# Kernel optimization log

Measured on AMD Instinct MI355X. Metric: run time of the kernel, lower is better.

Reference implementation:

```python
import jax, jax.numpy as jnp
import numpy as np

N, E, M, G = 100000, 1600000, 20000, 512
IN, ED, OUT, H, C = 64, 16, 64, 4, 8


def segment_softmax(alpha, seg, num):
    # alpha: [Etot, H]; softmax over edges sharing the same destination segment
    amax = jax.ops.segment_max(alpha, seg, num_segments=num)
    amax = jnp.where(jnp.isneginf(amax), 0.0, amax)
    ex = jnp.exp(alpha - amax[seg])
    den = jax.ops.segment_sum(ex, seg, num_segments=num)
    return ex / (den[seg] + 1e-16)


def gat_conv(x, src, dst, ea, W, We, a_s, a_d, a_e, b, concat):
    # PyG GATConv: shared lin for src/dst, edge-conditioned attention, self loops pre-added
    n = x.shape[0]
    h, c = a_s.shape
    hx = (x @ W).reshape(n, h, c)            # [N,H,C]
    ee = (ea @ We).reshape(-1, h, c)          # [Etot,H,C]
    alpha = jax.nn.leaky_relu((hx * a_s).sum(-1)[src] + (hx * a_d).sum(-1)[dst] + (ee * a_e).sum(-1), 0.2)
    alpha = segment_softmax(alpha, dst, n)    # [Etot,H]
    out = jax.ops.segment_sum(hx[src] * alpha[:, :, None], dst, num_segments=n)
    out = out.reshape(n, h * c) if concat else out.mean(axis=1)
    return out + b


def setup_inputs() -> dict:
    keys = iter(jax.random.split(jax.random.key(0), 64))

    def nrm(shape, s=0.1):
        return jax.random.normal(next(keys), shape, jnp.float32) * s

    inp = {}
    inp["x"] = jax.random.normal(next(keys), (N, IN), jnp.float32)
    inp["edge_index"] = jax.random.randint(next(keys), (2, E), 0, N)
    inp["edge_attr"] = jax.random.normal(next(keys), (E, ED), jnp.float32)
    inp["scatter_index"] = jax.random.randint(next(keys), (N,), 0, M)
    inp["scatter_norm"] = jax.random.uniform(next(keys), (M, 1), jnp.float32, 0.5, 2.0)
    inp["nodes"] = jax.random.randint(next(keys), (M,), 0, G)
    inp["decision_var_indexes"] = jax.random.randint(next(keys), (G,), 0, N)
    dims = [(IN, H, C), (H * C, H, C), (H * C, H, C), (H * C, H, OUT)]
    for i, (din, hh, cc) in enumerate(dims, 1):
        inp[f"W{i}"] = nrm((din, hh * cc))
        inp[f"We{i}"] = nrm((ED, hh * cc))
        inp[f"asrc{i}"] = nrm((hh, cc))
        inp[f"adst{i}"] = nrm((hh, cc))
        inp[f"ae{i}"] = nrm((hh, cc))
        inp[f"b{i}"] = nrm((hh * cc if i < 4 else cc,))
    inp["Wp"] = nrm((OUT, OUT))
    inp["Wt"] = nrm((OUT, OUT))
    inp["Wo"] = nrm((2 * OUT, 1))
    inp["bo"] = nrm((1,))
    return inp


def reference(x, edge_index, edge_attr, scatter_index, scatter_norm, nodes, decision_var_indexes,
              W1, We1, asrc1, adst1, ae1, b1, W2, We2, asrc2, adst2, ae2, b2,
              W3, We3, asrc3, adst3, ae3, b3, W4, We4, asrc4, adst4, ae4, b4,
              Wp, Wt, Wo, bo):
    # add self loops once; edge_attr fill_value='mean' (PyG GATConv default)
    loop = jnp.arange(N)
    src = jnp.concatenate([edge_index[0], loop])
    dst = jnp.concatenate([edge_index[1], loop])
    ea = jnp.concatenate([edge_attr, jnp.broadcast_to(edge_attr.mean(0), (N, ED))], 0)
    lrelu = lambda v: jax.nn.leaky_relu(v, 0.01)
    h1 = lrelu(gat_conv(x, src, dst, ea, W1, We1, asrc1, adst1, ae1, b1, True))
    h2 = lrelu(gat_conv(h1, src, dst, ea, W2, We2, asrc2, adst2, ae2, b2, True))
    h3 = lrelu(gat_conv(h2, src, dst, ea, W3, We3, asrc3, adst3, ae3, b3, True))
    h4 = lrelu(gat_conv(h3, src, dst, ea, W4, We4, asrc4, adst4, ae4, b4, False))
    pool = jax.ops.segment_sum(h4, scatter_index, num_segments=M) / scatter_norm
    pool = jax.ops.segment_sum(pool, nodes, num_segments=G)   # [G,OUT]
    tgt = h4[decision_var_indexes]                             # [G,OUT]
    feat = lrelu(jnp.concatenate([pool @ Wp, tgt @ Wt], axis=1))
    return feat @ Wo + bo
```

## Files before the change

kernel.cpp:

```cpp
#include <hip/hip_runtime.h>
#include <math.h>

#define NN 100000
#define EE 1600000
#define ETOT 1700000
#define MM 20000
#define GG 512

#define NBUCK 782
#define NB1 256
#define CAP 4096

static constexpr int NB_N256 = (NN + 255) / 256;
static constexpr int NB_E256 = (ETOT + 255) / 256;
static constexpr int NB_AGG  = NN / 32;

#define SM_MEAN 0
#define SM_WEA 16
#define SM_VS4 272
#define SM_VD4 400
#define SM_W4P 536
#define SM_TOTAL 8728

typedef unsigned long long ull;

__device__ __forceinline__ unsigned short f2bf(float f) {
  unsigned int u = __float_as_uint(f);
  u += 0x7fffu + ((u >> 16) & 1u);
  return (unsigned short)(u >> 16);
}
__device__ __forceinline__ float bf2f(unsigned int h) {
  return __uint_as_float(h << 16);
}
__device__ __forceinline__ float lrelu(float v, float s) { return v > 0.f ? v : s * v; }

__global__ __launch_bounds__(256) void k_pre(
    float* __restrict__ sm, const float* __restrict__ We1, const float* __restrict__ We2,
    const float* __restrict__ We3, const float* __restrict__ We4,
    const float* __restrict__ ae1, const float* __restrict__ ae2,
    const float* __restrict__ ae3, const float* __restrict__ ae4,
    const float* __restrict__ as4, const float* __restrict__ ad4,
    const float* __restrict__ W4) {
  int t = threadIdx.x;
  {
    int l = t >> 6, d = (t >> 2) & 15, h = t & 3;
    const float* We = (l == 0) ? We1 : (l == 1) ? We2 : (l == 2) ? We3 : We4;
    const float* ae = (l == 0) ? ae1 : (l == 1) ? ae2 : (l == 2) ? ae3 : ae4;
    int C = (l == 3) ? 64 : 8;
    float s = 0.f;
    for (int c = 0; c < C; c++) s += We[d * (4 * C) + h * C + c] * ae[h * C + c];
    sm[SM_WEA + l * 64 + d * 4 + h] = s;
  }
  if (t < 128) {
    int k = t >> 2, h = t & 3;
    float s1 = 0.f, s2 = 0.f;
    for (int c = 0; c < 64; c++) {
      float w = W4[k * 256 + h * 64 + c];
      s1 += w * as4[h * 64 + c];
      s2 += w * ad4[h * 64 + c];
    }
    sm[SM_VS4 + t] = s1;
    sm[SM_VD4 + t] = s2;
  }
  for (int i = t; i < 8192; i += 256) {
    int row = i >> 6, c = i & 63;
    int h = row >> 5, k = row & 31;
    sm[SM_W4P + i] = 0.25f * W4[k * 256 + h * 64 + c];
  }
}

__global__ __launch_bounds__(1024) void k_hist1(const int* __restrict__ ei,
                                                const float* __restrict__ ea,
                                                int* __restrict__ blk_cnt,
                                                float* __restrict__ sm) {
  __shared__ int hist[NBUCK];
  __shared__ float lsum[16];
  int t = threadIdx.x;
  for (int i = t; i < NBUCK; i += 1024) hist[i] = 0;
  if (t < 16) lsum[t] = 0.f;
  __syncthreads();
  for (int e = blockIdx.x * 1024 + t; e < ETOT; e += NB1 * 1024) {
    int dst = (e < EE) ? ei[EE + e] : (e - EE);
    atomicAdd(&hist[dst >> 7], 1);
  }
  {
    const float4* ea4 = (const float4*)ea;
    int q = t & 3;
    float4 a = make_float4(0.f, 0.f, 0.f, 0.f);
    for (size_t i = (size_t)blockIdx.x * 1024 + t; i < (size_t)EE * 4;
         i += (size_t)NB1 * 1024) {
      float4 v = ea4[i];
      a.x += v.x; a.y += v.y; a.z += v.z; a.w += v.w;
    }
    for (int m = 4; m < 64; m <<= 1) {
      a.x += __shfl_xor(a.x, m, 64);
      a.y += __shfl_xor(a.y, m, 64);
      a.z += __shfl_xor(a.z, m, 64);
      a.w += __shfl_xor(a.w, m, 64);
    }
    if ((t & 63) < 4) {
      atomicAdd(&lsum[q * 4 + 0], a.x);
      atomicAdd(&lsum[q * 4 + 1], a.y);
      atomicAdd(&lsum[q * 4 + 2], a.z);
      atomicAdd(&lsum[q * 4 + 3], a.w);
    }
  }
  __syncthreads();
  for (int i = t; i < NBUCK; i += 1024) blk_cnt[blockIdx.x * NBUCK + i] = hist[i];
  if (t < 16) atomicAdd(&sm[SM_MEAN + t], lsum[t]);
}

__global__ __launch_bounds__(256) void k_bscan_a(const int* __restrict__ blk_cnt,
                                                 int* __restrict__ blk_base_T,
                                                 int* __restrict__ bucket_tot) {
  __shared__ int s[256];
  int b = blockIdx.x, t = threadIdx.x;
  int v = blk_cnt[t * NBUCK + b];
  s[t] = v;
  __syncthreads();
  for (int off = 1; off < 256; off <<= 1) {
    int x = (t >= off) ? s[t - off] : 0;
    __syncthreads();
    s[t] += x;
    __syncthreads();
  }
  blk_base_T[b * 256 + t] = s[t] - v;
  if (t == 255) bucket_tot[b] = s[255];
}

__global__ __launch_bounds__(1024) void k_bscan_b(const int* __restrict__ bucket_tot,
                                                  int* __restrict__ bucket_base,
                                                  int* __restrict__ row_off) {
  __shared__ int s[1024];
  int t = threadIdx.x;
  int v = (t < NBUCK) ? bucket_tot[t] : 0;
  s[t] = v;
  __syncthreads();
  for (int off = 1; off < 1024; off <<= 1) {
    int x = (t >= off) ? s[t - off] : 0;
    __syncthreads();
    s[t] += x;
    __syncthreads();
  }
  if (t < NBUCK) bucket_base[t] = s[t] - v;
  if (t == 0) {
    bucket_base[NBUCK] = ETOT;
    row_off[NN] = ETOT;
  }
}

__global__ __launch_bounds__(1024) void k_scatter1(const int* __restrict__ ei,
                                                   const int* __restrict__ bucket_base,
                                                   const int* __restrict__ blk_base_T,
                                                   uint2* __restrict__ pairs) {
  __shared__ int base[NBUCK];
  __shared__ int rank[NBUCK];
  int t = threadIdx.x, blk = blockIdx.x;
  for (int i = t; i < NBUCK; i += 1024) {
    base[i] = bucket_base[i] + blk_base_T[i * 256 + blk];
    rank[i] = 0;
  }
  __syncthreads();
  for (int e = blk * 1024 + t; e < ETOT; e += NB1 * 1024) {
    int src, dst;
    if (e < EE) {
      src = ei[e];
      dst = ei[EE + e];
    } else {
      src = dst = e - EE;
    }
    int bin = dst >> 7;
    int r = atomicAdd(&rank[bin], 1);
    pairs[base[bin] + r] =
        make_uint2((unsigned)src, (unsigned)e | ((unsigned)(dst & 127) << 21));
  }
}

__global__ __launch_bounds__(256) void k_sort2(const uint2* __restrict__ pairs,
                                               const int* __restrict__ bucket_base,
                                               int* __restrict__ row_off,
                                               int* __restrict__ csr_src,
                                               int* __restrict__ eidx) {
  __shared__ uint2 plds[CAP];
  __shared__ unsigned short perm[CAP];
  __shared__ int hist[128];
  __shared__ int scan[128];
  __shared__ int rankv[128];
  int b = blockIdx.x, t = threadIdx.x;
  int start = bucket_base[b], end = bucket_base[b + 1];
  int cnt = end - start;
  if (t < 128) hist[t] = 0;
  __syncthreads();
  bool fits = (cnt <= CAP);
  if (fits) {
    for (int i = t; i < cnt; i += 256) {
      uint2 pe = pairs[start + i];
      plds[i] = pe;
      atomicAdd(&hist[(pe.y >> 21) & 127], 1);
    }
  } else {
    for (int i = t; i < cnt; i += 256)
      atomicAdd(&hist[(pairs[start + i].y >> 21) & 127], 1);
  }
  __syncthreads();
  if (t < 128) scan[t] = hist[t];
  __syncthreads();
  for (int off = 1; off < 128; off <<= 1) {
    int x = (t >= off && t < 128) ? scan[t - off] : 0;
    __syncthreads();
    if (t < 128) scan[t] += x;
    __syncthreads();
  }
  if (t < 128) {
    int excl = scan[t] - hist[t];
    rankv[t] = excl;
    int dst = b * 128 + t;
    if (dst < NN) row_off[dst] = start + excl;
  }
  __syncthreads();
  if (fits) {
    for (int i = t; i < cnt; i += 256) {
      int bin = (plds[i].y >> 21) & 127;
      int r = atomicAdd(&rankv[bin], 1);
      perm[r] = (unsigned short)i;
    }
    __syncthreads();
    for (int r = t; r < cnt; r += 256) {
      uint2 pe = plds[perm[r]];
      csr_src[start + r] = (int)pe.x;
      eidx[start + r] = (int)(pe.y & 0x1fffffu);
    }
  } else {
    for (int i = t; i < cnt; i += 256) {
      uint2 pe = pairs[start + i];
      int bin = (pe.y >> 21) & 127;
      int r = atomicAdd(&rankv[bin], 1);
      csr_src[start + r] = (int)pe.x;
      eidx[start + r] = (int)(pe.y & 0x1fffffu);
    }
  }
}

__global__ __launch_bounds__(256) void k_pack(const int* __restrict__ eidx,
                                              const float* __restrict__ ea,
                                              const float* __restrict__ sm,
                                              ull* __restrict__ apc) {
  __shared__ float sWea[256];
  __shared__ float smean[16];
  int t = threadIdx.x;
  sWea[t] = sm[SM_WEA + t];
  if (t < 16) smean[t] = sm[SM_MEAN + t] * (1.f / EE);
  __syncthreads();
  int pos = blockIdx.x * 256 + t;
  if (pos >= ETOT) return;
  int eid = eidx[pos];
  float eav[16];
  if (eid < EE) {
    const float4* p = (const float4*)(ea + (size_t)eid * 16);
    float4 v0 = p[0], v1 = p[1], v2 = p[2], v3 = p[3];
    eav[0] = v0.x; eav[1] = v0.y; eav[2] = v0.z; eav[3] = v0.w;
    eav[4] = v1.x; eav[5] = v1.y; eav[6] = v1.z; eav[7] = v1.w;
    eav[8] = v2.x; eav[9] = v2.y; eav[10] = v2.z; eav[11] = v2.w;
    eav[12] = v3.x; eav[13] = v3.y; eav[14] = v3.z; eav[15] = v3.w;
  } else {
#pragma unroll
    for (int d = 0; d < 16; d++) eav[d] = smean[d];
  }
#pragma unroll
  for (int l = 0; l < 4; l++) {
    ull pk = 0;
#pragma unroll
    for (int h = 0; h < 4; h++) {
      float s = 0.f;
#pragma unroll
      for (int d = 0; d < 16; d++) s += eav[d] * sWea[l * 64 + d * 4 + h];
      pk |= (ull)f2bf(s) << (16 * h);
    }
    apc[(size_t)l * ETOT + pos] = pk;
  }
}

template <int DIN>
__global__ __launch_bounds__(256) void k_t(const float* __restrict__ in,
                                           const float* __restrict__ W,
                                           const float* __restrict__ a_s,
                                           const float* __restrict__ a_d,
                                           unsigned short* __restrict__ hxb,
                                           float* __restrict__ ssrc,
                                           float* __restrict__ sdst) {
  __shared__ float4 sW[DIN * 8];
  __shared__ float sas[32], sad[32];
  int t = threadIdx.x;
  for (int i = t; i < DIN * 8; i += 256) sW[i] = ((const float4*)W)[i];
  if (t < 32) { sas[t] = a_s[t]; sad[t] = a_d[t]; }
  __syncthreads();
  int n = blockIdx.x * 256 + t;
  if (n >= NN) return;
  float acc[32];
#pragma unroll
  for (int j = 0; j < 32; j++) acc[j] = 0.f;
  const float* xr = in + (size_t)n * DIN;
  for (int k = 0; k < DIN; k += 4) {
    float4 xv = *(const float4*)(xr + k);
    float xa[4] = {xv.x, xv.y, xv.z, xv.w};
#pragma unroll
    for (int kk = 0; kk < 4; kk++) {
#pragma unroll
      for (int j4 = 0; j4 < 8; j4++) {
        float4 ww = sW[(k + kk) * 8 + j4];
        acc[j4 * 4 + 0] += xa[kk] * ww.x;
        acc[j4 * 4 + 1] += xa[kk] * ww.y;
        acc[j4 * 4 + 2] += xa[kk] * ww.z;
        acc[j4 * 4 + 3] += xa[kk] * ww.w;
      }
    }
  }
  float ssum[4], dsum[4];
#pragma unroll
  for (int h = 0; h < 4; h++) {
    float s = 0.f, d = 0.f;
#pragma unroll
    for (int c = 0; c < 8; c++) {
      s += acc[h * 8 + c] * sas[h * 8 + c];
      d += acc[h * 8 + c] * sad[h * 8 + c];
    }
    ssum[h] = s;
    dsum[h] = d;
  }
  unsigned int up[16];
#pragma unroll
  for (int i = 0; i < 16; i++)
    up[i] = (unsigned)f2bf(acc[2 * i]) | ((unsigned)f2bf(acc[2 * i + 1]) << 16);
  uint4* ho = (uint4*)(hxb + (size_t)n * 32);
  ho[0] = make_uint4(up[0], up[1], up[2], up[3]);
  ho[1] = make_uint4(up[4], up[5], up[6], up[7]);
  ho[2] = make_uint4(up[8], up[9], up[10], up[11]);
  ho[3] = make_uint4(up[12], up[13], up[14], up[15]);
  ((float4*)ssrc)[n] = make_float4(ssum[0], ssum[1], ssum[2], ssum[3]);
  ((float4*)sdst)[n] = make_float4(dsum[0], dsum[1], dsum[2], dsum[3]);
}

__global__ __launch_bounds__(256) void k_aggt(const int* __restrict__ row_off,
                                              const int* __restrict__ csr_src,
                                              const ull* __restrict__ apl,
                                              const unsigned short* __restrict__ hxb,
                                              const float* __restrict__ ssrc,
                                              const float* __restrict__ sdst,
                                              const float* __restrict__ bias,
                                              const float* __restrict__ Wn,
                                              const float* __restrict__ asn,
                                              const float* __restrict__ adn,
                                              unsigned short* __restrict__ hxb_out,
                                              float* __restrict__ ssrc_out,
                                              float* __restrict__ sdst_out) {
  __shared__ float4 sW[256];
  __shared__ float sas[32], sad[32];
  int t = threadIdx.x;
  sW[t] = ((const float4*)Wn)[t];
  if (t < 32) { sas[t] = asn[t]; sad[t] = adn[t]; }
  __syncthreads();
  int g = t >> 3, j = t & 7, h = j >> 1;
  int n = blockIdx.x * 32 + g;
  float sd = sdst[n * 4 + h];
  int e0 = row_off[n], e1 = row_off[n + 1];
  float den = 0.f;
  float4 acc = make_float4(0.f, 0.f, 0.f, 0.f);
  int e = e0;
  for (; e + 8 <= e1; e += 8) {
    int s[8];
    ull p[8];
#pragma unroll
    for (int k = 0; k < 8; k++) s[k] = csr_src[e + k];
#pragma unroll
    for (int k = 0; k < 8; k++) p[k] = apl[e + k];
    float a[8];
    uint2 u[8];
#pragma unroll
    for (int k = 0; k < 8; k++) a[k] = ssrc[s[k] * 4 + h];
#pragma unroll
    for (int k = 0; k < 8; k++)
      u[k] = *(const uint2*)(hxb + (size_t)s[k] * 32 + (j << 2));
#pragma unroll
    for (int k = 0; k < 8; k++) {
      float al = a[k] + sd + bf2f((unsigned)(unsigned short)(p[k] >> (16 * h)));
      float q = __expf(fminf(lrelu(al, 0.2f), 80.f));
      den += q;
      acc.x += q * bf2f(u[k].x & 0xffffu);
      acc.y += q * bf2f(u[k].x >> 16);
      acc.z += q * bf2f(u[k].y & 0xffffu);
      acc.w += q * bf2f(u[k].y >> 16);
    }
  }
  for (; e + 4 <= e1; e += 4) {
    int s[4];
    ull p[4];
#pragma unroll
    for (int k = 0; k < 4; k++) s[k] = csr_src[e + k];
#pragma unroll
    for (int k = 0; k < 4; k++) p[k] = apl[e + k];
    float a[4];
    uint2 u[4];
#pragma unroll
    for (int k = 0; k < 4; k++) a[k] = ssrc[s[k] * 4 + h];
#pragma unroll
    for (int k = 0; k < 4; k++)
      u[k] = *(const uint2*)(hxb + (size_t)s[k] * 32 + (j << 2));
#pragma unroll
    for (int k = 0; k < 4; k++) {
      float al = a[k] + sd + bf2f((unsigned)(unsigned short)(p[k] >> (16 * h)));
      float q = __expf(fminf(lrelu(al, 0.2f), 80.f));
      den += q;
      acc.x += q * bf2f(u[k].x & 0xffffu);
      acc.y += q * bf2f(u[k].x >> 16);
      acc.z += q * bf2f(u[k].y & 0xffffu);
      acc.w += q * bf2f(u[k].y >> 16);
    }
  }
  for (; e < e1; ++e) {
    int src = csr_src[e];
    ull pk = apl[e];
    float al = ssrc[src * 4 + h] + sd + bf2f((unsigned)(unsigned short)(pk >> (16 * h)));
    al = fminf(lrelu(al, 0.2f), 80.f);
    uint2 u = *(const uint2*)(hxb + (size_t)src * 32 + (j << 2));
    float p = __expf(al);
    den += p;
    acc.x += p * bf2f(u.x & 0xffffu);
    acc.y += p * bf2f(u.x >> 16);
    acc.z += p * bf2f(u.y & 0xffffu);
    acc.w += p * bf2f(u.y >> 16);
  }
  float inv = 1.f / (den + 1e-16f);
  float4 b = *(const float4*)(bias + (j << 2));
  float i0 = lrelu(acc.x * inv + b.x, 0.01f);
  float i1 = lrelu(acc.y * inv + b.y, 0.01f);
  float i2 = lrelu(acc.z * inv + b.z, 0.01f);
  float i3 = lrelu(acc.w * inv + b.w, 0.01f);
  int gbase = (t & 63) & ~7;
  float n0 = 0.f, n1 = 0.f, n2 = 0.f, n3 = 0.f;
#pragma unroll
  for (int k = 0; k < 8; k++) {
    int sl = gbase + k;
    float v0 = __shfl(i0, sl, 64);
    float v1 = __shfl(i1, sl, 64);
    float v2 = __shfl(i2, sl, 64);
    float v3 = __shfl(i3, sl, 64);
    float4 w0 = sW[(k * 4 + 0) * 8 + j];
    n0 += v0 * w0.x; n1 += v0 * w0.y; n2 += v0 * w0.z; n3 += v0 * w0.w;
    float4 w1 = sW[(k * 4 + 1) * 8 + j];
    n0 += v1 * w1.x; n1 += v1 * w1.y; n2 += v1 * w1.z; n3 += v1 * w1.w;
    float4 w2 = sW[(k * 4 + 2) * 8 + j];
    n0 += v2 * w2.x; n1 += v2 * w2.y; n2 += v2 * w2.z; n3 += v2 * w2.w;
    float4 w3 = sW[(k * 4 + 3) * 8 + j];
    n0 += v3 * w3.x; n1 += v3 * w3.y; n2 += v3 * w3.z; n3 += v3 * w3.w;
  }
  float ps = n0 * sas[j * 4 + 0] + n1 * sas[j * 4 + 1] + n2 * sas[j * 4 + 2] +
             n3 * sas[j * 4 + 3];
  float pd = n0 * sad[j * 4 + 0] + n1 * sad[j * 4 + 1] + n2 * sad[j * 4 + 2] +
             n3 * sad[j * 4 + 3];
  ps += __shfl_xor(ps, 1, 64);
  pd += __shfl_xor(pd, 1, 64);
  if ((j & 1) == 0) {
    ssrc_out[n * 4 + (j >> 1)] = ps;
    sdst_out[n * 4 + (j >> 1)] = pd;
  }
  unsigned u0 = (unsigned)f2bf(n0) | ((unsigned)f2bf(n1) << 16);
  unsigned u1 = (unsigned)f2bf(n2) | ((unsigned)f2bf(n3) << 16);
  *(uint2*)(hxb_out + (size_t)n * 32 + (j << 2)) = make_uint2(u0, u1);
}

__global__ __launch_bounds__(256) void k_aggt3(const int* __restrict__ row_off,
                                               const int* __restrict__ csr_src,
                                               const ull* __restrict__ apl,
                                               const unsigned short* __restrict__ hxb,
                                               const float* __restrict__ ssrc,
                                               const float* __restrict__ sdst,
                                               const float* __restrict__ bias,
                                               const float* __restrict__ sm,
                                               unsigned short* __restrict__ h3b,
                                               float* __restrict__ ssrc4,
                                               float* __restrict__ sdst4) {
  __shared__ float sVs[128], sVd[128];
  int t = threadIdx.x;
  if (t < 128) { sVs[t] = sm[SM_VS4 + t]; sVd[t] = sm[SM_VD4 + t]; }
  __syncthreads();
  int g = t >> 3, j = t & 7, h = j >> 1;
  int n = blockIdx.x * 32 + g;
  float sd = sdst[n * 4 + h];
  int e0 = row_off[n], e1 = row_off[n + 1];
  float den = 0.f;
  float4 acc = make_float4(0.f, 0.f, 0.f, 0.f);
  int e = e0;
  for (; e + 8 <= e1; e += 8) {
    int s[8];
    ull p[8];
#pragma unroll
    for (int k = 0; k < 8; k++) s[k] = csr_src[e + k];
#pragma unroll
    for (int k = 0; k < 8; k++) p[k] = apl[e + k];
    float a[8];
    uint2 u[8];
#pragma unroll
    for (int k = 0; k < 8; k++) a[k] = ssrc[s[k] * 4 + h];
#pragma unroll
    for (int k = 0; k < 8; k++)
      u[k] = *(const uint2*)(hxb + (size_t)s[k] * 32 + (j << 2));
#pragma unroll
    for (int k = 0; k < 8; k++) {
      float al = a[k] + sd + bf2f((unsigned)(unsigned short)(p[k] >> (16 * h)));
      float q = __expf(fminf(lrelu(al, 0.2f), 80.f));
      den += q;
      acc.x += q * bf2f(u[k].x & 0xffffu);
      acc.y += q * bf2f(u[k].x >> 16);
      acc.z += q * bf2f(u[k].y & 0xffffu);
      acc.w += q * bf2f(u[k].y >> 16);
    }
  }
  for (; e + 4 <= e1; e += 4) {
    int s[4];
    ull p[4];
#pragma unroll
    for (int k = 0; k < 4; k++) s[k] = csr_src[e + k];
#pragma unroll
    for (int k = 0; k < 4; k++) p[k] = apl[e + k];
    float a[4];
    uint2 u[4];
#pragma unroll
    for (int k = 0; k < 4; k++) a[k] = ssrc[s[k] * 4 + h];
#pragma unroll
    for (int k = 0; k < 4; k++)
      u[k] = *(const uint2*)(hxb + (size_t)s[k] * 32 + (j << 2));
#pragma unroll
    for (int k = 0; k < 4; k++) {
      float al = a[k] + sd + bf2f((unsigned)(unsigned short)(p[k] >> (16 * h)));
      float q = __expf(fminf(lrelu(al, 0.2f), 80.f));
      den += q;
      acc.x += q * bf2f(u[k].x & 0xffffu);
      acc.y += q * bf2f(u[k].x >> 16);
      acc.z += q * bf2f(u[k].y & 0xffffu);
      acc.w += q * bf2f(u[k].y >> 16);
    }
  }
  for (; e < e1; ++e) {
    int src = csr_src[e];
    ull pk = apl[e];
    float al = ssrc[src * 4 + h] + sd + bf2f((unsigned)(unsigned short)(pk >> (16 * h)));
    al = fminf(lrelu(al, 0.2f), 80.f);
    uint2 u = *(const uint2*)(hxb + (size_t)src * 32 + (j << 2));
    float p = __expf(al);
    den += p;
    acc.x += p * bf2f(u.x & 0xffffu);
    acc.y += p * bf2f(u.x >> 16);
    acc.z += p * bf2f(u.y & 0xffffu);
    acc.w += p * bf2f(u.y >> 16);
  }
  float inv = 1.f / (den + 1e-16f);
  float4 b = *(const float4*)(bias + (j << 2));
  float o0 = lrelu(acc.x * inv + b.x, 0.01f);
  float o1 = lrelu(acc.y * inv + b.y, 0.01f);
  float o2 = lrelu(acc.z * inv + b.z, 0.01f);
  float o3 = lrelu(acc.w * inv + b.w, 0.01f);
  float ps0 = o0 * sVs[(j * 4 + 0) * 4 + 0] + o1 * sVs[(j * 4 + 1) * 4 + 0] +
              o2 * sVs[(j * 4 + 2) * 4 + 0] + o3 * sVs[(j * 4 + 3) * 4 + 0];
  float ps1 = o0 * sVs[(j * 4 + 0) * 4 + 1] + o1 * sVs[(j * 4 + 1) * 4 + 1] +
              o2 * sVs[(j * 4 + 2) * 4 + 1] + o3 * sVs[(j * 4 + 3) * 4 + 1];
  float ps2 = o0 * sVs[(j * 4 + 0) * 4 + 2] + o1 * sVs[(j * 4 + 1) * 4 + 2] +
              o2 * sVs[(j * 4 + 2) * 4 + 2] + o3 * sVs[(j * 4 + 3) * 4 + 2];
  float ps3 = o0 * sVs[(j * 4 + 0) * 4 + 3] + o1 * sVs[(j * 4 + 1) * 4 + 3] +
              o2 * sVs[(j * 4 + 2) * 4 + 3] + o3 * sVs[(j * 4 + 3) * 4 + 3];
  float pd0 = o0 * sVd[(j * 4 + 0) * 4 + 0] + o1 * sVd[(j * 4 + 1) * 4 + 0] +
              o2 * sVd[(j * 4 + 2) * 4 + 0] + o3 * sVd[(j * 4 + 3) * 4 + 0];
  float pd1 = o0 * sVd[(j * 4 + 0) * 4 + 1] + o1 * sVd[(j * 4 + 1) * 4 + 1] +
              o2 * sVd[(j * 4 + 2) * 4 + 1] + o3 * sVd[(j * 4 + 3) * 4 + 1];
  float pd2 = o0 * sVd[(j * 4 + 0) * 4 + 2] + o1 * sVd[(j * 4 + 1) * 4 + 2] +
              o2 * sVd[(j * 4 + 2) * 4 + 2] + o3 * sVd[(j * 4 + 3) * 4 + 2];
  float pd3 = o0 * sVd[(j * 4 + 0) * 4 + 3] + o1 * sVd[(j * 4 + 1) * 4 + 3] +
              o2 * sVd[(j * 4 + 2) * 4 + 3] + o3 * sVd[(j * 4 + 3) * 4 + 3];
#pragma unroll
  for (int m = 1; m < 8; m <<= 1) {
    ps0 += __shfl_xor(ps0, m, 64);
    ps1 += __shfl_xor(ps1, m, 64);
    ps2 += __shfl_xor(ps2, m, 64);
    ps3 += __shfl_xor(ps3, m, 64);
    pd0 += __shfl_xor(pd0, m, 64);
    pd1 += __shfl_xor(pd1, m, 64);
    pd2 += __shfl_xor(pd2, m, 64);
    pd3 += __shfl_xor(pd3, m, 64);
  }
  if (j == 0) {
    ((float4*)ssrc4)[n] = make_float4(ps0, ps1, ps2, ps3);
    ((float4*)sdst4)[n] = make_float4(pd0, pd1, pd2, pd3);
  }
  unsigned u0 = (unsigned)f2bf(o0) | ((unsigned)f2bf(o1) << 16);
  unsigned u1 = (unsigned)f2bf(o2) | ((unsigned)f2bf(o3) << 16);
  *(uint2*)(h3b + (size_t)n * 32 + (j << 2)) = make_uint2(u0, u1);
}

__global__ __launch_bounds__(256) void k_agg4(const int* __restrict__ row_off,
                                              const int* __restrict__ csr_src,
                                              const ull* __restrict__ apl,
                                              const unsigned short* __restrict__ h3b,
                                              const float* __restrict__ ssrc,
                                              const float* __restrict__ sdst,
                                              unsigned short* __restrict__ aggb) {
  int t = threadIdx.x;
  int g = t >> 3, j = t & 7;
  int n = blockIdx.x * 32 + g;
  if (n >= NN) return;
  float4 sdv = ((const float4*)sdst)[n];
  float sda[4] = {sdv.x, sdv.y, sdv.z, sdv.w};
  int e0 = row_off[n], e1 = row_off[n + 1];
  float den[4];
  float4 acc[4];
#pragma unroll
  for (int h = 0; h < 4; h++) {
    den[h] = 0.f;
    acc[h] = make_float4(0.f, 0.f, 0.f, 0.f);
  }
  int e = e0;
  for (; e + 4 <= e1; e += 4) {
    int s[4];
    ull p[4];
#pragma unroll
    for (int k = 0; k < 4; k++) s[k] = csr_src[e + k];
#pragma unroll
    for (int k = 0; k < 4; k++) p[k] = apl[e + k];
    float4 sv[4];
    uint2 u[4];
#pragma unroll
    for (int k = 0; k < 4; k++) sv[k] = ((const float4*)ssrc)[s[k]];
#pragma unroll
    for (int k = 0; k < 4; k++)
      u[k] = *(const uint2*)(h3b + (size_t)s[k] * 32 + (j << 2));
#pragma unroll
    for (int k = 0; k < 4; k++) {
      float x0 = bf2f(u[k].x & 0xffffu), x1 = bf2f(u[k].x >> 16);
      float x2 = bf2f(u[k].y & 0xffffu), x3 = bf2f(u[k].y >> 16);
      float sa[4] = {sv[k].x, sv[k].y, sv[k].z, sv[k].w};
#pragma unroll
      for (int h = 0; h < 4; h++) {
        float al = sa[h] + sda[h] + bf2f((unsigned)(unsigned short)(p[k] >> (16 * h)));
        float q = __expf(fminf(lrelu(al, 0.2f), 80.f));
        den[h] += q;
        acc[h].x += q * x0;
        acc[h].y += q * x1;
        acc[h].z += q * x2;
        acc[h].w += q * x3;
      }
    }
  }
  for (; e < e1; ++e) {
    int src = csr_src[e];
    ull pk = apl[e];
    float4 ssv = ((const float4*)ssrc)[src];
    float ssa[4] = {ssv.x, ssv.y, ssv.z, ssv.w};
    uint2 u = *(const uint2*)(h3b + (size_t)src * 32 + (j << 2));
    float hx0 = bf2f(u.x & 0xffffu), hx1 = bf2f(u.x >> 16);
    float hx2 = bf2f(u.y & 0xffffu), hx3 = bf2f(u.y >> 16);
#pragma unroll
    for (int h = 0; h < 4; h++) {
      float al = ssa[h] + sda[h] + bf2f((unsigned)(unsigned short)(pk >> (16 * h)));
      al = fminf(lrelu(al, 0.2f), 80.f);
      float p = __expf(al);
      den[h] += p;
      acc[h].x += p * hx0;
      acc[h].y += p * hx1;
      acc[h].z += p * hx2;
      acc[h].w += p * hx3;
    }
  }
#pragma unroll
  for (int h = 0; h < 4; h++) {
    float inv = 1.f / (den[h] + 1e-16f);
    unsigned int u0 = (unsigned)f2bf(acc[h].x * inv) | ((unsigned)f2bf(acc[h].y * inv) << 16);
    unsigned int u1 = (unsigned)f2bf(acc[h].z * inv) | ((unsigned)f2bf(acc[h].w * inv) << 16);
    *(uint2*)(aggb + (size_t)n * 128 + h * 32 + (j << 2)) = make_uint2(u0, u1);
  }
}

__global__ __launch_bounds__(256) void k_epi4(const unsigned short* __restrict__ aggb,
                                              const float* __restrict__ sm,
                                              const float* __restrict__ b4,
                                              float* __restrict__ h4) {
  __shared__ float4 sW[2048];
  __shared__ float sb[64];
  int t = threadIdx.x;
  for (int i = t; i < 2048; i += 256) sW[i] = ((const float4*)(sm + SM_W4P))[i];
  if (t < 64) sb[t] = b4[t];
  __syncthreads();
  int n = blockIdx.x * 256 + t;
  if (n >= NN) return;
  float acc[64];
#pragma unroll
  for (int j = 0; j < 64; j++) acc[j] = 0.f;
  const unsigned short* r = aggb + (size_t)n * 128;
  for (int k = 0; k < 128; k += 4) {
    uint2 u = *(const uint2*)(r + k);
    float va[4] = {bf2f(u.x & 0xffffu), bf2f(u.x >> 16), bf2f(u.y & 0xffffu),
                   bf2f(u.y >> 16)};
#pragma unroll
    for (int kk = 0; kk < 4; kk++) {
#pragma unroll
      for (int j4 = 0; j4 < 16; j4++) {
        float4 wv = sW[(k + kk) * 16 + j4];
        acc[j4 * 4 + 0] += va[kk] * wv.x;
        acc[j4 * 4 + 1] += va[kk] * wv.y;
        acc[j4 * 4 + 2] += va[kk] * wv.z;
        acc[j4 * 4 + 3] += va[kk] * wv.w;
      }
    }
  }
  float* o = h4 + (size_t)n * 64;
#pragma unroll
  for (int j4 = 0; j4 < 16; j4++) {
    float4 ov;
    ov.x = lrelu(acc[j4 * 4 + 0] + sb[j4 * 4 + 0], 0.01f);
    ov.y = lrelu(acc[j4 * 4 + 1] + sb[j4 * 4 + 1], 0.01f);
    ov.z = lrelu(acc[j4 * 4 + 2] + sb[j4 * 4 + 2], 0.01f);
    ov.w = lrelu(acc[j4 * 4 + 3] + sb[j4 * 4 + 3], 0.01f);
    ((float4*)o)[j4] = ov;
  }
}

__global__ __launch_bounds__(256) void k_pool1(const float* __restrict__ h4,
                                               const int* __restrict__ sidx,
                                               float* __restrict__ pool1) {
  int i = blockIdx.x * 256 + threadIdx.x;
  if (i >= NN * 64) return;
  int n = i >> 6, c = i & 63;
  atomicAdd(&pool1[(size_t)sidx[n] * 64 + c], h4[i]);
}

__global__ __launch_bounds__(256) void k_pool2(const float* __restrict__ pool1,
                                               const float* __restrict__ snorm,
                                               const int* __restrict__ nodes,
                                               float* __restrict__ pool2) {
  int i = blockIdx.x * 256 + threadIdx.x;
  if (i >= MM * 64) return;
  int mi = i >> 6, c = i & 63;
  float v = pool1[i] / snorm[mi];
  atomicAdd(&pool2[(size_t)nodes[mi] * 64 + c], v);
}

__global__ __launch_bounds__(64) void k_final(const float* __restrict__ pool2,
                                              const float* __restrict__ h4,
                                              const int* __restrict__ dvi,
                                              const float* __restrict__ Wp,
                                              const float* __restrict__ Wt,
                                              const float* __restrict__ Wo,
                                              const float* __restrict__ bo,
                                              float* __restrict__ out) {
  __shared__ float p[64], tt[64];
  int gI = blockIdx.x, j = threadIdx.x;
  p[j] = pool2[gI * 64 + j];
  tt[j] = h4[(size_t)dvi[gI] * 64 + j];
  __syncthreads();
  float f1 = 0.f, f2 = 0.f;
#pragma unroll 8
  for (int c = 0; c < 64; c++) {
    f1 += p[c] * Wp[c * 64 + j];
    f2 += tt[c] * Wt[c * 64 + j];
  }
  f1 = lrelu(f1, 0.01f);
  f2 = lrelu(f2, 0.01f);
  float v = f1 * Wo[j] + f2 * Wo[64 + j];
  for (int off = 32; off > 0; off >>= 1) v += __shfl_down(v, off, 64);
  if (j == 0) out[gI] = v + bo[0];
}

extern "C" void kernel_launch(void* const* d_in, const int* in_sizes, int n_in,
                              void* d_out, int out_size, void* d_ws, size_t ws_size,
                              hipStream_t stream) {
  const float* x = (const float*)d_in[0];
  const int* ei = (const int*)d_in[1];
  const float* ea = (const float*)d_in[2];
  const int* sidx = (const int*)d_in[3];
  const float* snorm = (const float*)d_in[4];
  const int* nodes = (const int*)d_in[5];
  const int* dvi = (const int*)d_in[6];
  const float* W1 = (const float*)d_in[7];
  const float* as1 = (const float*)d_in[9];
  const float* ad1 = (const float*)d_in[10];
  const float* b1 = (const float*)d_in[12];
  const float* W2 = (const float*)d_in[13];
  const float* as2 = (const float*)d_in[15];
  const float* ad2 = (const float*)d_in[16];
  const float* b2 = (const float*)d_in[18];
  const float* W3 = (const float*)d_in[19];
  const float* as3 = (const float*)d_in[21];
  const float* ad3 = (const float*)d_in[22];
  const float* b3 = (const float*)d_in[24];
  const float* b4 = (const float*)d_in[30];
  const float* Wp = (const float*)d_in[31];
  const float* Wt = (const float*)d_in[32];
  const float* Wo = (const float*)d_in[33];
  const float* bo = (const float*)d_in[34];
  float* out = (float*)d_out;

  char* w = (char*)d_ws;
  size_t off = 0;
  auto take = [&](size_t bytes) -> char* {
    char* p = w + off;
    off = (off + bytes + 255) & ~(size_t)255;
    return p;
  };
  int* row_off = (int*)take((size_t)(NN + 1) * 4);
  float* sm = (float*)take(SM_TOTAL * 4);
  uint2* pairs = (uint2*)take((size_t)ETOT * 8);
  int* csr_src = (int*)take((size_t)ETOT * 4);
  int* eidx = (int*)take((size_t)ETOT * 4);
  ull* apc = (ull*)take((size_t)ETOT * 4 * 8);
  int* blk_cnt = (int*)take((size_t)NB1 * NBUCK * 4);
  int* blk_base_T = (int*)take((size_t)NBUCK * NB1 * 4);
  int* bucket_tot = (int*)take((size_t)NBUCK * 4);
  int* bucket_base = (int*)take((size_t)(NBUCK + 1) * 4);
  float* h4 = (float*)take((size_t)NN * 64 * 4);
  unsigned short* aggb = (unsigned short*)take((size_t)NN * 128 * 2);
  unsigned short* hxbA = (unsigned short*)take((size_t)NN * 32 * 2);
  unsigned short* hxbB = (unsigned short*)take((size_t)NN * 32 * 2);
  unsigned short* h3b = (unsigned short*)take((size_t)NN * 32 * 2);
  float* ssrcA = (float*)take((size_t)NN * 4 * 4);
  float* sdstA = (float*)take((size_t)NN * 4 * 4);
  float* ssrcB = (float*)take((size_t)NN * 4 * 4);
  float* sdstB = (float*)take((size_t)NN * 4 * 4);
  float* ssrc4 = (float*)take((size_t)NN * 4 * 4);
  float* sdst4 = (float*)take((size_t)NN * 4 * 4);
  float* pool1 = (float*)take((size_t)MM * 64 * 4);
  float* pool2 = (float*)take((size_t)GG * 64 * 4);
  if (off > ws_size) return;

  hipMemsetAsync(sm, 0, 64, stream);
  hipMemsetAsync(pool1, 0, (size_t)MM * 64 * 4, stream);
  hipMemsetAsync(pool2, 0, (size_t)GG * 64 * 4, stream);

  k_pre<<<1, 256, 0, stream>>>(sm, (const float*)d_in[8], (const float*)d_in[14],
                               (const float*)d_in[20], (const float*)d_in[26],
                               (const float*)d_in[11], (const float*)d_in[17],
                               (const float*)d_in[23], (const float*)d_in[29],
                               (const float*)d_in[27], (const float*)d_in[28],
                               (const float*)d_in[25]);

  k_hist1<<<NB1, 1024, 0, stream>>>(ei, ea, blk_cnt, sm);
  k_bscan_a<<<NBUCK, 256, 0, stream>>>(blk_cnt, blk_base_T, bucket_tot);
  k_bscan_b<<<1, 1024, 0, stream>>>(bucket_tot, bucket_base, row_off);
  k_scatter1<<<NB1, 1024, 0, stream>>>(ei, bucket_base, blk_base_T, pairs);
  k_sort2<<<NBUCK, 256, 0, stream>>>(pairs, bucket_base, row_off, csr_src, eidx);
  k_pack<<<NB_E256, 256, 0, stream>>>(eidx, ea, sm, apc);

  k_t<64><<<NB_N256, 256, 0, stream>>>(x, W1, as1, ad1, hxbA, ssrcA, sdstA);
  k_aggt<<<NB_AGG, 256, 0, stream>>>(row_off, csr_src, apc, hxbA, ssrcA, sdstA, b1, W2,
                                     as2, ad2, hxbB, ssrcB, sdstB);
  k_aggt<<<NB_AGG, 256, 0, stream>>>(row_off, csr_src, apc + (size_t)ETOT, hxbB, ssrcB,
                                     sdstB, b2, W3, as3, ad3, hxbA, ssrcA, sdstA);
  k_aggt3<<<NB_AGG, 256, 0, stream>>>(row_off, csr_src, apc + 2 * (size_t)ETOT, hxbA,
                                      ssrcA, sdstA, b3, sm, h3b, ssrc4, sdst4);
  k_agg4<<<NB_AGG, 256, 0, stream>>>(row_off, csr_src, apc + 3 * (size_t)ETOT, h3b,
                                     ssrc4, sdst4, aggb);
  k_epi4<<<NB_N256, 256, 0, stream>>>(aggb, sm, b4, h4);

  k_pool1<<<(NN * 64) / 256, 256, 0, stream>>>(h4, sidx, pool1);
  k_pool2<<<(MM * 64) / 256, 256, 0, stream>>>(pool1, snorm, nodes, pool2);
  k_final<<<GG, 64, 0, stream>>>(pool2, h4, dvi, Wp, Wt, Wo, bo, out);
}
```

Before: 621.0 us.

## Fuse edge-attr mean into pack, patch self-loops later, fuse pool1 into epilogue

The edge_attr column-sum moves out of the histogram kernel into k_pack, which reduces the edge features it already loads, so edge_attr is read once instead of twice. Self-loop attention terms are then written by two small kernels (k_selfpack, k_selffix) using self-loop CSR positions recorded during the sort. The layer-4 epilogue atomically accumulates into pool1 directly and writes h4 only for rows marked as decision-variable targets, which removes the separate k_pool1 pass and most h4 stores. The cost is three extra tiny launches and per-thread float atomics on pool1 rows instead of coalesced element-wise atomics.

```diff
diff --git a/kernel.cpp b/kernel.cpp
--- a/kernel.cpp
+++ b/kernel.cpp
@@ -19,6 +19,7 @@
 #define SM_WEA 16
 #define SM_VS4 272
 #define SM_VD4 400
+#define SM_SELF 528
 #define SM_W4P 536
 #define SM_TOTAL 8728
 
@@ -70,44 +71,17 @@
 }
 
 __global__ __launch_bounds__(1024) void k_hist1(const int* __restrict__ ei,
-                                                const float* __restrict__ ea,
-                                                int* __restrict__ blk_cnt,
-                                                float* __restrict__ sm) {
+                                                int* __restrict__ blk_cnt) {
   __shared__ int hist[NBUCK];
-  __shared__ float lsum[16];
   int t = threadIdx.x;
   for (int i = t; i < NBUCK; i += 1024) hist[i] = 0;
-  if (t < 16) lsum[t] = 0.f;
   __syncthreads();
   for (int e = blockIdx.x * 1024 + t; e < ETOT; e += NB1 * 1024) {
     int dst = (e < EE) ? ei[EE + e] : (e - EE);
     atomicAdd(&hist[dst >> 7], 1);
   }
-  {
-    const float4* ea4 = (const float4*)ea;
-    int q = t & 3;
-    float4 a = make_float4(0.f, 0.f, 0.f, 0.f);
-    for (size_t i = (size_t)blockIdx.x * 1024 + t; i < (size_t)EE * 4;
-         i += (size_t)NB1 * 1024) {
-      float4 v = ea4[i];
-      a.x += v.x; a.y += v.y; a.z += v.z; a.w += v.w;
-    }
-    for (int m = 4; m < 64; m <<= 1) {
-      a.x += __shfl_xor(a.x, m, 64);
-      a.y += __shfl_xor(a.y, m, 64);
-      a.z += __shfl_xor(a.z, m, 64);
-      a.w += __shfl_xor(a.w, m, 64);
-    }
-    if ((t & 63) < 4) {
-      atomicAdd(&lsum[q * 4 + 0], a.x);
-      atomicAdd(&lsum[q * 4 + 1], a.y);
-      atomicAdd(&lsum[q * 4 + 2], a.z);
-      atomicAdd(&lsum[q * 4 + 3], a.w);
-    }
-  }
   __syncthreads();
   for (int i = t; i < NBUCK; i += 1024) blk_cnt[blockIdx.x * NBUCK + i] = hist[i];
-  if (t < 16) atomicAdd(&sm[SM_MEAN + t], lsum[t]);
 }
 
 __global__ __launch_bounds__(256) void k_bscan_a(const int* __restrict__ blk_cnt,
@@ -180,7 +154,8 @@
                                                const int* __restrict__ bucket_base,
                                                int* __restrict__ row_off,
                                                int* __restrict__ csr_src,
-                                               int* __restrict__ eidx) {
+                                               int* __restrict__ eidx,
+                                               int* __restrict__ selfpos) {
   __shared__ uint2 plds[CAP];
   __shared__ unsigned short perm[CAP];
   __shared__ int hist[128];
@@ -227,57 +202,112 @@
     __syncthreads();
     for (int r = t; r < cnt; r += 256) {
       uint2 pe = plds[perm[r]];
+      unsigned eid = pe.y & 0x1fffffu;
       csr_src[start + r] = (int)pe.x;
-      eidx[start + r] = (int)(pe.y & 0x1fffffu);
+      eidx[start + r] = (int)eid;
+      if (eid >= EE) selfpos[b * 128 + ((pe.y >> 21) & 127)] = start + r;
     }
   } else {
     for (int i = t; i < cnt; i += 256) {
       uint2 pe = pairs[start + i];
       int bin = (pe.y >> 21) & 127;
+      unsigned eid = pe.y & 0x1fffffu;
       int r = atomicAdd(&rankv[bin], 1);
       csr_src[start + r] = (int)pe.x;
-      eidx[start + r] = (int)(pe.y & 0x1fffffu);
+      eidx[start + r] = (int)eid;
+      if (eid >= EE) selfpos[b * 128 + bin] = start + r;
     }
   }
 }
 
 __global__ __launch_bounds__(256) void k_pack(const int* __restrict__ eidx,
                                               const float* __restrict__ ea,
-                                              const float* __restrict__ sm,
+                                              float* __restrict__ sm,
                                               ull* __restrict__ apc) {
   __shared__ float sWea[256];
-  __shared__ float smean[16];
+  __shared__ float lsum[16];
   int t = threadIdx.x;
   sWea[t] = sm[SM_WEA + t];
-  if (t < 16) smean[t] = sm[SM_MEAN + t] * (1.f / EE);
+  if (t < 16) lsum[t] = 0.f;
   __syncthreads();
   int pos = blockIdx.x * 256 + t;
-  if (pos >= ETOT) return;
-  int eid = eidx[pos];
   float eav[16];
-  if (eid < EE) {
-    const float4* p = (const float4*)(ea + (size_t)eid * 16);
-    float4 v0 = p[0], v1 = p[1], v2 = p[2], v3 = p[3];
-    eav[0] = v0.x; eav[1] = v0.y; eav[2] = v0.z; eav[3] = v0.w;
-    eav[4] = v1.x; eav[5] = v1.y; eav[6] = v1.z; eav[7] = v1.w;
-    eav[8] = v2.x; eav[9] = v2.y; eav[10] = v2.z; eav[11] = v2.w;
-    eav[12] = v3.x; eav[13] = v3.y; eav[14] = v3.z; eav[15] = v3.w;
-  } else {
-#pragma unroll
-    for (int d = 0; d < 16; d++) eav[d] = smean[d];
-  }
-#pragma unroll
-  for (int l = 0; l < 4; l++) {
+#pragma unroll
+  for (int d = 0; d < 16; d++) eav[d] = 0.f;
+  bool real = false;
+  if (pos < ETOT) {
+    int eid = eidx[pos];
+    if (eid < EE) {
+      real = true;
+      const float4* p = (const float4*)(ea + (size_t)eid * 16);
+      float4 v0 = p[0], v1 = p[1], v2 = p[2], v3 = p[3];
+      eav[0] = v0.x; eav[1] = v0.y; eav[2] = v0.z; eav[3] = v0.w;
+      eav[4] = v1.x; eav[5] = v1.y; eav[6] = v1.z; eav[7] = v1.w;
+      eav[8] = v2.x; eav[9] = v2.y; eav[10] = v2.z; eav[11] = v2.w;
+      eav[12] = v3.x; eav[13] = v3.y; eav[14] = v3.z; eav[15] = v3.w;
+    }
+  }
+  if (real) {
+#pragma unroll
+    for (int l = 0; l < 4; l++) {
+      ull pk = 0;
+#pragma unroll
+      for (int h = 0; h < 4; h++) {
+        float s = 0.f;
+#pragma unroll
+        for (int d = 0; d < 16; d++) s += eav[d] * sWea[l * 64 + d * 4 + h];
+        pk |= (ull)f2bf(s) << (16 * h);
+      }
+      apc[(size_t)l * ETOT + pos] = pk;
+    }
+  }
+#pragma unroll
+  for (int d = 0; d < 16; d++) {
+    float v = eav[d];
+    for (int m = 1; m < 64; m <<= 1) v += __shfl_xor(v, m, 64);
+    eav[d] = v;
+  }
+  if ((t & 63) == 0) {
+#pragma unroll
+    for (int d = 0; d < 16; d++) atomicAdd(&lsum[d], eav[d]);
+  }
+  __syncthreads();
+  if (t < 16) atomicAdd(&sm[SM_MEAN + t], lsum[t]);
+}
+
+__global__ __launch_bounds__(64) void k_selfpack(float* __restrict__ sm) {
+  int t = threadIdx.x;
+  if (t < 16) sm[SM_MEAN + t] *= (1.f / EE);
+  __syncthreads();
+  if (t < 4) {
     ull pk = 0;
-#pragma unroll
     for (int h = 0; h < 4; h++) {
       float s = 0.f;
-#pragma unroll
-      for (int d = 0; d < 16; d++) s += eav[d] * sWea[l * 64 + d * 4 + h];
+      for (int d = 0; d < 16; d++) s += sm[SM_MEAN + d] * sm[SM_WEA + t * 64 + d * 4 + h];
       pk |= (ull)f2bf(s) << (16 * h);
     }
-    apc[(size_t)l * ETOT + pos] = pk;
-  }
+    ((ull*)(sm + SM_SELF))[t] = pk;
+  }
+}
+
+__global__ __launch_bounds__(256) void k_selffix(const int* __restrict__ selfpos,
+                                                 const float* __restrict__ sm,
+                                                 ull* __restrict__ apc) {
+  int n = blockIdx.x * 256 + threadIdx.x;
+  if (n >= NN) return;
+  int pos = selfpos[n];
+  const ull* sp = (const ull*)(sm + SM_SELF);
+  ull p0 = sp[0], p1 = sp[1], p2 = sp[2], p3 = sp[3];
+  apc[pos] = p0;
+  apc[(size_t)ETOT + pos] = p1;
+  apc[2 * (size_t)ETOT + pos] = p2;
+  apc[3 * (size_t)ETOT + pos] = p3;
+}
+
+__global__ __launch_bounds__(256) void k_mark(const int* __restrict__ dvi,
+                                              char* __restrict__ mark) {
+  int i = blockIdx.x * 256 + threadIdx.x;
+  if (i < GG) mark[dvi[i]] = 1;
 }
 
 template <int DIN>
@@ -677,10 +707,13 @@
   }
 }
 
-__global__ __launch_bounds__(256) void k_epi4(const unsigned short* __restrict__ aggb,
-                                              const float* __restrict__ sm,
-                                              const float* __restrict__ b4,
-                                              float* __restrict__ h4) {
+__global__ __launch_bounds__(256) void k_epi4p(const unsigned short* __restrict__ aggb,
+                                               const float* __restrict__ sm,
+                                               const float* __restrict__ b4,
+                                               const int* __restrict__ sidx,
+                                               const char* __restrict__ mark,
+                                               float* __restrict__ pool1,
+                                               float* __restrict__ h4) {
   __shared__ float4 sW[2048];
   __shared__ float sb[64];
   int t = threadIdx.x;
@@ -709,6 +742,8 @@
       }
     }
   }
+  float* prow = pool1 + (size_t)sidx[n] * 64;
+  bool wr = mark[n] != 0;
   float* o = h4 + (size_t)n * 64;
 #pragma unroll
   for (int j4 = 0; j4 < 16; j4++) {
@@ -717,17 +752,12 @@
     ov.y = lrelu(acc[j4 * 4 + 1] + sb[j4 * 4 + 1], 0.01f);
     ov.z = lrelu(acc[j4 * 4 + 2] + sb[j4 * 4 + 2], 0.01f);
     ov.w = lrelu(acc[j4 * 4 + 3] + sb[j4 * 4 + 3], 0.01f);
-    ((float4*)o)[j4] = ov;
-  }
-}
-
-__global__ __launch_bounds__(256) void k_pool1(const float* __restrict__ h4,
-                                               const int* __restrict__ sidx,
-                                               float* __restrict__ pool1) {
-  int i = blockIdx.x * 256 + threadIdx.x;
-  if (i >= NN * 64) return;
-  int n = i >> 6, c = i & 63;
-  atomicAdd(&pool1[(size_t)sidx[n] * 64 + c], h4[i]);
+    atomicAdd(&prow[j4 * 4 + 0], ov.x);
+    atomicAdd(&prow[j4 * 4 + 1], ov.y);
+    atomicAdd(&prow[j4 * 4 + 2], ov.z);
+    atomicAdd(&prow[j4 * 4 + 3], ov.w);
+    if (wr) ((float4*)o)[j4] = ov;
+  }
 }
 
 __global__ __launch_bounds__(256) void k_pool2(const float* __restrict__ pool1,
@@ -813,6 +843,8 @@
   int* blk_base_T = (int*)take((size_t)NBUCK * NB1 * 4);
   int* bucket_tot = (int*)take((size_t)NBUCK * 4);
   int* bucket_base = (int*)take((size_t)(NBUCK + 1) * 4);
+  int* selfpos = (int*)take((size_t)NN * 4);
+  char* mark = (char*)take((size_t)NN);
   float* h4 = (float*)take((size_t)NN * 64 * 4);
   unsigned short* aggb = (unsigned short*)take((size_t)NN * 128 * 2);
   unsigned short* hxbA = (unsigned short*)take((size_t)NN * 32 * 2);
@@ -829,6 +861,7 @@
   if (off > ws_size) return;
 
   hipMemsetAsync(sm, 0, 64, stream);
+  hipMemsetAsync(mark, 0, (size_t)NN, stream);
   hipMemsetAsync(pool1, 0, (size_t)MM * 64 * 4, stream);
   hipMemsetAsync(pool2, 0, (size_t)GG * 64 * 4, stream);
 
@@ -838,13 +871,17 @@
                                (const float*)d_in[23], (const float*)d_in[29],
                                (const float*)d_in[27], (const float*)d_in[28],
                                (const float*)d_in[25]);
-
-  k_hist1<<<NB1, 1024, 0, stream>>>(ei, ea, blk_cnt, sm);
+  k_mark<<<2, 256, 0, stream>>>(dvi, mark);
+
+  k_hist1<<<NB1, 1024, 0, stream>>>(ei, blk_cnt);
   k_bscan_a<<<NBUCK, 256, 0, stream>>>(blk_cnt, blk_base_T, bucket_tot);
   k_bscan_b<<<1, 1024, 0, stream>>>(bucket_tot, bucket_base, row_off);
   k_scatter1<<<NB1, 1024, 0, stream>>>(ei, bucket_base, blk_base_T, pairs);
-  k_sort2<<<NBUCK, 256, 0, stream>>>(pairs, bucket_base, row_off, csr_src, eidx);
+  k_sort2<<<NBUCK, 256, 0, stream>>>(pairs, bucket_base, row_off, csr_src, eidx,
+                                     selfpos);
   k_pack<<<NB_E256, 256, 0, stream>>>(eidx, ea, sm, apc);
+  k_selfpack<<<1, 64, 0, stream>>>(sm);
+  k_selffix<<<NB_N256, 256, 0, stream>>>(selfpos, sm, apc);
 
   k_t<64><<<NB_N256, 256, 0, stream>>>(x, W1, as1, ad1, hxbA, ssrcA, sdstA);
   k_aggt<<<NB_AGG, 256, 0, stream>>>(row_off, csr_src, apc, hxbA, ssrcA, sdstA, b1, W2,
@@ -855,9 +892,8 @@
                                       ssrcA, sdstA, b3, sm, h3b, ssrc4, sdst4);
   k_agg4<<<NB_AGG, 256, 0, stream>>>(row_off, csr_src, apc + 3 * (size_t)ETOT, h3b,
                                      ssrc4, sdst4, aggb);
-  k_epi4<<<NB_N256, 256, 0, stream>>>(aggb, sm, b4, h4);
-
-  k_pool1<<<(NN * 64) / 256, 256, 0, stream>>>(h4, sidx, pool1);
+  k_epi4p<<<NB_N256, 256, 0, stream>>>(aggb, sm, b4, sidx, mark, pool1, h4);
+
   k_pool2<<<(MM * 64) / 256, 256, 0, stream>>>(pool1, snorm, nodes, pool2);
   k_final<<<GG, 64, 0, stream>>>(pool2, h4, dvi, Wp, Wt, Wo, bo, out);
 }
```

Result: slower. 1.141 ms (+83.7%).
